# Performance work log

Hardware: AMD Instinct MI355X
Metric: run time of the kernel (lower is better)

Reference implementation:

```python
import math
import jax, jax.numpy as jnp
import numpy as np

B, Q, K, D = 32, 1024, 1024, 128
MASK_VALUE = -1000000.0


def setup_inputs() -> dict:
    key = jax.random.key(0)
    kq, kk, kv, kl = jax.random.split(key, 4)
    return {
        "queries": jax.random.normal(kq, (B, Q, D), dtype=jnp.float32),
        "keys": jax.random.normal(kk, (B, K, D), dtype=jnp.float32),
        "values": jax.random.normal(kv, (B, K, D), dtype=jnp.float32),
        "valid_lens": jax.random.randint(kl, (B,), 1, K + 1, dtype=jnp.int32),
    }


def reference(queries, keys, values, valid_lens):
    d = queries.shape[-1]
    # scores: [B, Q, K]
    scores = jnp.einsum("bqd,bkd->bqk", queries, keys) / math.sqrt(d)
    # key-padding mask: position k valid iff k < valid_lens[b] (broadcast over queries)
    mask = jnp.arange(keys.shape[1])[None, None, :] < valid_lens[:, None, None]
    scores = jnp.where(mask, scores, MASK_VALUE)
    attn = jax.nn.softmax(scores, axis=-1)
    # dropout p=0.0 -> identity
    return jnp.einsum("bqk,bkv->bqv", attn, values)
```

## Files before the change

kernel.cpp:

```cpp
#include <hip/hip_runtime.h>
#include <math.h>

typedef _Float16 f16;
typedef __attribute__((ext_vector_type(8))) _Float16 f16x8;
typedef __attribute__((ext_vector_type(4))) _Float16 f16x4;
typedef __attribute__((ext_vector_type(4))) float f32x4;

constexpr int BATCH = 32;
constexpr int QL = 1024;
constexpr int KL = 1024;
constexpr int D = 128;
constexpr int BQ = 64;
constexpr int BK = 64;
constexpr int CT = 8;
constexpr int DKP = 136;
constexpr int BKP = 72;

#define CSC 0.12752863187087177f

static __device__ __forceinline__ f16x4 pk4(float x, float y, float z, float w) {
  auto a = __builtin_amdgcn_cvt_pkrtz(x, y);
  auto b = __builtin_amdgcn_cvt_pkrtz(z, w);
  f16x4 h;
  h[0] = (f16)a[0]; h[1] = (f16)a[1]; h[2] = (f16)b[0]; h[3] = (f16)b[1];
  return h;
}
static __device__ __forceinline__ f16x8 pk8(float4 u, float4 v) {
  f16x4 a = pk4(u.x, u.y, u.z, u.w);
  f16x4 b = pk4(v.x, v.y, v.z, v.w);
  f16x8 h;
  h[0] = a[0]; h[1] = a[1]; h[2] = a[2]; h[3] = a[3];
  h[4] = b[0]; h[5] = b[1]; h[6] = b[2]; h[7] = b[3];
  return h;
}
static __device__ __forceinline__ f16x8 pk8v(f32x4 a, f32x4 b) {
  auto x0 = __builtin_amdgcn_cvt_pkrtz(a[0], a[1]);
  auto x1 = __builtin_amdgcn_cvt_pkrtz(a[2], a[3]);
  auto x2 = __builtin_amdgcn_cvt_pkrtz(b[0], b[1]);
  auto x3 = __builtin_amdgcn_cvt_pkrtz(b[2], b[3]);
  f16x8 h;
  h[0] = x0[0]; h[1] = x0[1]; h[2] = x1[0]; h[3] = x1[1];
  h[4] = x2[0]; h[5] = x2[1]; h[6] = x3[0]; h[7] = x3[1];
  return h;
}
static __device__ __forceinline__ f16x8 pk8s(float4 u, float4 v) {
  float4 a = {u.x * CSC, u.y * CSC, u.z * CSC, u.w * CSC};
  float4 b = {v.x * CSC, v.y * CSC, v.z * CSC, v.w * CSC};
  return pk8(a, b);
}

static __device__ __forceinline__ int krp(int kk) {
  return ((kk >> 5) << 5) | (((kk >> 2) & 1) << 4) | (((kk >> 3) & 3) << 2) | (kk & 3);
}

#define ISSUE(KR, VR, T)                                                   \
  do {                                                                     \
    const float4* Kt = (const float4*)(Kb + (size_t)(T) * BK * D);         \
    _Pragma("unroll")                                                      \
    for (int i_ = 0; i_ < 4; ++i_) {                                       \
      int cc_ = tid + i_ * 256;                                            \
      int row_ = cc_ >> 4, d04_ = (cc_ & 15) * 2;                          \
      KR[2 * i_]     = Kt[row_ * 32 + d04_];                               \
      KR[2 * i_ + 1] = Kt[row_ * 32 + d04_ + 1];                           \
    }                                                                      \
    const float* Vt = Vb + (size_t)(T) * BK * D;                           \
    _Pragma("unroll")                                                      \
    for (int i_ = 0; i_ < 2; ++i_) {                                       \
      int f_ = tid + i_ * 256;                                             \
      const float* base_ = Vt + (size_t)((f_ & 15) * 4) * D + (f_ >> 4) * 4; \
      VR[i_ * 4 + 0] = *(const float4*)(base_);                            \
      VR[i_ * 4 + 1] = *(const float4*)(base_ + D);                        \
      VR[i_ * 4 + 2] = *(const float4*)(base_ + 2 * D);                    \
      VR[i_ * 4 + 3] = *(const float4*)(base_ + 3 * D);                    \
    }                                                                      \
  } while (0)

#define DRAIN(KR, VR)                                                      \
  do {                                                                     \
    _Pragma("unroll")                                                      \
    for (int i_ = 0; i_ < 4; ++i_) {                                       \
      int cc_ = tid + i_ * 256;                                            \
      int row_ = cc_ >> 4, d0_ = (cc_ & 15) * 8;                           \
      *(f16x8*)&sK[krp(row_)][d0_] = pk8(KR[2 * i_], KR[2 * i_ + 1]);      \
    }                                                                      \
    _Pragma("unroll")                                                      \
    for (int i_ = 0; i_ < 2; ++i_) {                                       \
      int f_ = tid + i_ * 256;                                             \
      int k0_ = (f_ & 15) * 4, d0_ = (f_ >> 4) * 4;                        \
      float4 r0_ = VR[i_*4+0], r1_ = VR[i_*4+1], r2_ = VR[i_*4+2], r3_ = VR[i_*4+3]; \
      *(f16x4*)&sVT[d0_ + 0][k0_] = pk4(r0_.x, r1_.x, r2_.x, r3_.x);       \
      *(f16x4*)&sVT[d0_ + 1][k0_] = pk4(r0_.y, r1_.y, r2_.y, r3_.y);       \
      *(f16x4*)&sVT[d0_ + 2][k0_] = pk4(r0_.z, r1_.z, r2_.z, r3_.z);       \
      *(f16x4*)&sVT[d0_ + 3][k0_] = pk4(r0_.w, r1_.w, r2_.w, r3_.w);       \
    }                                                                      \
  } while (0)

#define TILE_BARRIER()                                                     \
  do {                                                                     \
    asm volatile("s_waitcnt lgkmcnt(0)" ::: "memory");                     \
    __builtin_amdgcn_s_barrier();                                          \
    asm volatile("" ::: "memory");                                         \
  } while (0)

__global__ __launch_bounds__(256, 2)
void attn_fwd(const float* __restrict__ Qp, const float* __restrict__ Kp,
              const float* __restrict__ Vp, const int* __restrict__ VLp,
              float* __restrict__ Op, float* __restrict__ wsO,
              float* __restrict__ wsL, int nks) {
  __shared__ f16 sK[BK][DKP];
  __shared__ f16 sVT[D][BKP];
  __shared__ int sN[32];
  __shared__ int sI[32];
  __shared__ int sCost[8];
  __shared__ int sCls[8];

  const int tid  = threadIdx.x;
  const int wave = tid >> 6, lane = tid & 63;
  const int l16  = lane & 15, quad = lane >> 4;

  if (tid < 32) sN[tid] = (VLp[tid] + BK - 1) / BK;
  __syncthreads();
  if (tid < 32) {
    int nb = sN[tid], r = 0;
    #pragma unroll
    for (int k = 0; k < 32; ++k) {
      int nk = sN[k];
      r += (nk > nb) || (nk == nb && k < tid);
    }
    sI[r] = tid;
  }
  __syncthreads();

  const int xcd = blockIdx.x & 7;
  const int j   = (int)blockIdx.x >> 3;

  int b, qt, ks, t0, t1, nt, vl;
  if (nks == 2) {
    if (tid < 8) {
      int lb = tid >> 1, kss = tid & 1;
      int gr = (lb == 0) ? xcd : (lb == 1) ? (15 - xcd)
             : (lb == 2) ? (16 + xcd) : (31 - xcd);
      int ntb = sN[sI[gr]];
      sCost[tid] = kss ? max(ntb - CT, 0) : min(ntb, CT);
    }
    __syncthreads();
    if (tid < 8) {
      int c = sCost[tid], r = 0;
      #pragma unroll
      for (int k = 0; k < 8; ++k)
        r += (sCost[k] > c) || (sCost[k] == c && k < tid);
      sCls[r] = tid;
    }
    __syncthreads();
    const int slot = j >> 5, c31 = j & 31;
    const int r = (slot == 0) ? c31 : (slot == 1) ? (63 - c31)
                : (slot == 2) ? (64 + c31) : (127 - c31);
    const int cls = sCls[r >> 4];
    const int lb = cls >> 1;
    ks = cls & 1;
    qt = r & 15;
    const int gr = (lb == 0) ? xcd : (lb == 1) ? (15 - xcd)
                 : (lb == 2) ? (16 + xcd) : (31 - xcd);
    b  = sI[gr];
    vl = VLp[b];
    nt = (vl + BK - 1) / BK;
    t0 = ks * CT;
    t1 = min(nt, ks * CT + CT);
    if (t0 >= t1) return;
  } else {
    const int jj = (j < 32) ? j : (95 - j);
    const int lr = jj >> 4;
    qt = jj & 15;
    ks = 0;
    const int gr = (lr == 0) ? xcd : (lr == 1) ? (15 - xcd)
                 : (lr == 2) ? (16 + xcd) : (31 - xcd);
    b  = sI[gr];
    vl = VLp[b];
    nt = (vl + BK - 1) / BK;
    t0 = 0; t1 = nt;
  }

  const float* Kb = Kp + (size_t)b * KL * D;
  const float* Vb = Vp + (size_t)b * KL * D;

  float4 kreg[8], vreg[8];

  const float* Qb = Qp + ((size_t)(b * QL + qt * BQ + wave * 16 + l16)) * D;
  float4 qtmp[8];
  #pragma unroll
  for (int kc = 0; kc < 4; ++kc) {
    const float* p = Qb + kc * 32 + quad * 8;
    qtmp[2 * kc]     = *(const float4*)p;
    qtmp[2 * kc + 1] = *(const float4*)(p + 4);
  }

  ISSUE(kreg, vreg, t0);

  f16x8 qf[4];
  #pragma unroll
  for (int kc = 0; kc < 4; ++kc) qf[kc] = pk8s(qtmp[2 * kc], qtmp[2 * kc + 1]);

  float lsum = 0.f;
  f32x4 o[8];
  #pragma unroll
  for (int dt = 0; dt < 8; ++dt) o[dt] = (f32x4){0.f, 0.f, 0.f, 0.f};

  for (int t = t0; t < t1; ++t) {
    TILE_BARRIER();
    DRAIN(kreg, vreg);
    if (t + 1 < t1) ISSUE(kreg, vreg, t + 1);
    TILE_BARRIER();

    f32x4 sv[4];
    #pragma unroll
    for (int ct = 0; ct < 4; ++ct) {
      f32x4 cacc = (f32x4){0.f, 0.f, 0.f, 0.f};
      #pragma unroll
      for (int kc = 0; kc < 4; ++kc) {
        f16x8 kf = *(const f16x8*)&sK[ct * 16 + l16][kc * 32 + quad * 8];
        cacc = __builtin_amdgcn_mfma_f32_16x16x32_f16(kf, qf[kc], cacc, 0, 0, 0);
      }
      sv[ct] = cacc;
    }

    if (t * BK + BK > vl) {
      #pragma unroll
      for (int ct = 0; ct < 4; ++ct) {
        int kb = t * BK + (ct >> 1) * 32 + (ct & 1) * 4 + quad * 8;
        #pragma unroll
        for (int r = 0; r < 4; ++r)
          sv[ct][r] = (kb + r) < vl ? sv[ct][r] : -1.0e9f;
      }
    }

    #pragma unroll
    for (int ct = 0; ct < 4; ++ct) {
      #pragma unroll
      for (int r = 0; r < 4; ++r) {
        float p = __builtin_amdgcn_exp2f(sv[ct][r]);
        sv[ct][r] = p;
        lsum += p;
      }
    }
    f16x8 pf0 = pk8v(sv[0], sv[1]);
    f16x8 pf1 = pk8v(sv[2], sv[3]);

    #pragma unroll
    for (int dt = 0; dt < 8; ++dt) {
      f16x8 vf0 = *(const f16x8*)&sVT[dt * 16 + l16][quad * 8];
      o[dt] = __builtin_amdgcn_mfma_f32_16x16x32_f16(vf0, pf0, o[dt], 0, 0, 0);
      f16x8 vf1 = *(const f16x8*)&sVT[dt * 16 + l16][32 + quad * 8];
      o[dt] = __builtin_amdgcn_mfma_f32_16x16x32_f16(vf1, pf1, o[dt], 0, 0, 0);
    }
  }

  float ls = lsum;
  ls += __shfl_xor(ls, 16);
  ls += __shfl_xor(ls, 32);

  if (nks == 1 || nt <= CT) {
    float* Ob = Op + ((size_t)(b * QL + qt * BQ + wave * 16)) * D;
    const float inv = 1.0f / ls;
    #pragma unroll
    for (int dt = 0; dt < 8; ++dt) {
      float4 w = {o[dt][0] * inv, o[dt][1] * inv, o[dt][2] * inv, o[dt][3] * inv};
      *(float4*)&Ob[(size_t)l16 * D + dt * 16 + quad * 4] = w;
    }
  } else {
    const int pair = b * 16 + qt;
    float* dst = (ks == 0)
        ? Op + ((size_t)(b * QL + qt * BQ + wave * 16)) * D
        : wsO + (size_t)pair * BQ * D + (size_t)(wave * 16) * D;
    #pragma unroll
    for (int dt = 0; dt < 8; ++dt) {
      float4 w = {o[dt][0], o[dt][1], o[dt][2], o[dt][3]};
      *(float4*)&dst[(size_t)l16 * D + dt * 16 + quad * 4] = w;
    }
    if (quad == 0) wsL[(pair * 2 + ks) * 64 + wave * 16 + l16] = ls;
  }
}

__global__ __launch_bounds__(256)
void attn_combine(float* __restrict__ Op, const float* __restrict__ wsO,
                  const float* __restrict__ wsL, const int* __restrict__ VLp) {
  const int pair = blockIdx.x;
  const int b = pair >> 4;
  if (VLp[b] <= CT * BK) return;
  float* Ob = Op + ((size_t)(b * QL + (pair & 15) * BQ)) * D;
  const float* o1 = wsO + (size_t)pair * BQ * D;
  const float* Lt = wsL + pair * 128;
  const int tid = threadIdx.x;
  #pragma unroll
  for (int i = 0; i < 8; ++i) {
    int fi = tid + i * 256;
    int row = fi >> 5;
    float inv = 1.0f / (Lt[row] + Lt[64 + row]);
    float4 a = ((const float4*)Ob)[fi];
    float4 c = ((const float4*)o1)[fi];
    float4 w = {(a.x + c.x) * inv, (a.y + c.y) * inv,
                (a.z + c.z) * inv, (a.w + c.w) * inv};
    ((float4*)Ob)[fi] = w;
  }
}

extern "C" void kernel_launch(void* const* d_in, const int* in_sizes, int n_in,
                              void* d_out, int out_size, void* d_ws, size_t ws_size,
                              hipStream_t stream) {
  const float* Qp = (const float*)d_in[0];
  const float* Kp = (const float*)d_in[1];
  const float* Vp = (const float*)d_in[2];
  const int*   VL = (const int*)d_in[3];
  float* Op = (float*)d_out;

  const size_t n_pairs = (size_t)BATCH * (QL / BQ);
  const size_t need = n_pairs * BQ * D * 4 + n_pairs * 128 * 4;
  if (d_ws != nullptr && ws_size >= need) {
    float* wsO = (float*)d_ws;
    float* wsL = (float*)d_ws + n_pairs * BQ * D;
    attn_fwd<<<dim3(2 * (int)n_pairs), dim3(256), 0, stream>>>(
        Qp, Kp, Vp, VL, Op, wsO, wsL, 2);
    attn_combine<<<dim3((int)n_pairs), dim3(256), 0, stream>>>(Op, wsO, wsL, VL);
  } else {
    attn_fwd<<<dim3((int)n_pairs), dim3(256), 0, stream>>>(
        Qp, Kp, Vp, VL, Op, nullptr, nullptr, 1);
  }
}
```

Before: 124.9 us.

## Generalize split-K to four key chunks and drop cost-sorted block scheduling

Generalizes the flash-attention key split from a fixed two chunks to a runtime count (four when the workspace allows), each block covering 16/nks key tiles, and the combine kernel sums a variable number of partial outputs and row sums. It also replaces the per-block cost ranking of (batch, split) classes with a plain index mapping. The aim is finer-grained work units, so that batches with very different valid lengths balance better across CUs. In exchange the combine pass reads more workspace traffic and many more, smaller blocks are launched, most of which exit early.

```diff
diff --git a/kernel.cpp b/kernel.cpp
--- a/kernel.cpp
+++ b/kernel.cpp
@@ -12,7 +12,6 @@
 constexpr int D = 128;
 constexpr int BQ = 64;
 constexpr int BK = 64;
-constexpr int CT = 8;
 constexpr int DKP = 136;
 constexpr int BKP = 72;
 
@@ -111,12 +110,11 @@
   __shared__ f16 sVT[D][BKP];
   __shared__ int sN[32];
   __shared__ int sI[32];
-  __shared__ int sCost[8];
-  __shared__ int sCls[8];
 
   const int tid  = threadIdx.x;
   const int wave = tid >> 6, lane = tid & 63;
   const int l16  = lane & 15, quad = lane >> 4;
+  const int ctk  = 16 / nks;
 
   if (tid < 32) sN[tid] = (VLp[tid] + BK - 1) / BK;
   __syncthreads();
@@ -135,37 +133,17 @@
   const int j   = (int)blockIdx.x >> 3;
 
   int b, qt, ks, t0, t1, nt, vl;
-  if (nks == 2) {
-    if (tid < 8) {
-      int lb = tid >> 1, kss = tid & 1;
-      int gr = (lb == 0) ? xcd : (lb == 1) ? (15 - xcd)
-             : (lb == 2) ? (16 + xcd) : (31 - xcd);
-      int ntb = sN[sI[gr]];
-      sCost[tid] = kss ? max(ntb - CT, 0) : min(ntb, CT);
-    }
-    __syncthreads();
-    if (tid < 8) {
-      int c = sCost[tid], r = 0;
-      #pragma unroll
-      for (int k = 0; k < 8; ++k)
-        r += (sCost[k] > c) || (sCost[k] == c && k < tid);
-      sCls[r] = tid;
-    }
-    __syncthreads();
-    const int slot = j >> 5, c31 = j & 31;
-    const int r = (slot == 0) ? c31 : (slot == 1) ? (63 - c31)
-                : (slot == 2) ? (64 + c31) : (127 - c31);
-    const int cls = sCls[r >> 4];
-    const int lb = cls >> 1;
-    ks = cls & 1;
-    qt = r & 15;
+  if (nks >= 2) {
+    ks = j >> 6;
+    const int lb = (j >> 4) & 3;
+    qt = j & 15;
     const int gr = (lb == 0) ? xcd : (lb == 1) ? (15 - xcd)
                  : (lb == 2) ? (16 + xcd) : (31 - xcd);
     b  = sI[gr];
     vl = VLp[b];
     nt = (vl + BK - 1) / BK;
-    t0 = ks * CT;
-    t1 = min(nt, ks * CT + CT);
+    t0 = ks * ctk;
+    t1 = min(nt, t0 + ctk);
     if (t0 >= t1) return;
   } else {
     const int jj = (j < 32) ? j : (95 - j);
@@ -258,7 +236,7 @@
   ls += __shfl_xor(ls, 16);
   ls += __shfl_xor(ls, 32);
 
-  if (nks == 1 || nt <= CT) {
+  if (nks == 1 || nt <= ctk) {
     float* Ob = Op + ((size_t)(b * QL + qt * BQ + wave * 16)) * D;
     const float inv = 1.0f / ls;
     #pragma unroll
@@ -270,35 +248,45 @@
     const int pair = b * 16 + qt;
     float* dst = (ks == 0)
         ? Op + ((size_t)(b * QL + qt * BQ + wave * 16)) * D
-        : wsO + (size_t)pair * BQ * D + (size_t)(wave * 16) * D;
+        : wsO + ((size_t)pair * (nks - 1) + (ks - 1)) * BQ * D
+              + (size_t)(wave * 16) * D;
     #pragma unroll
     for (int dt = 0; dt < 8; ++dt) {
       float4 w = {o[dt][0], o[dt][1], o[dt][2], o[dt][3]};
       *(float4*)&dst[(size_t)l16 * D + dt * 16 + quad * 4] = w;
     }
-    if (quad == 0) wsL[(pair * 2 + ks) * 64 + wave * 16 + l16] = ls;
+    if (quad == 0) wsL[(pair * nks + ks) * 64 + wave * 16 + l16] = ls;
   }
 }
 
 __global__ __launch_bounds__(256)
 void attn_combine(float* __restrict__ Op, const float* __restrict__ wsO,
-                  const float* __restrict__ wsL, const int* __restrict__ VLp) {
+                  const float* __restrict__ wsL, const int* __restrict__ VLp,
+                  int nks) {
   const int pair = blockIdx.x;
   const int b = pair >> 4;
-  if (VLp[b] <= CT * BK) return;
+  const int ctk = 16 / nks;
+  const int nt = (VLp[b] + BK - 1) / BK;
+  if (nt <= ctk) return;
+  const int nch = (nt + ctk - 1) / ctk;
   float* Ob = Op + ((size_t)(b * QL + (pair & 15) * BQ)) * D;
-  const float* o1 = wsO + (size_t)pair * BQ * D;
-  const float* Lt = wsL + pair * 128;
+  const float* Lt = wsL + (size_t)pair * nks * 64;
   const int tid = threadIdx.x;
   #pragma unroll
   for (int i = 0; i < 8; ++i) {
     int fi = tid + i * 256;
     int row = fi >> 5;
-    float inv = 1.0f / (Lt[row] + Lt[64 + row]);
+    float l = Lt[row];
+    for (int p = 1; p < nch; ++p) l += Lt[p * 64 + row];
+    float inv = 1.0f / l;
     float4 a = ((const float4*)Ob)[fi];
-    float4 c = ((const float4*)o1)[fi];
-    float4 w = {(a.x + c.x) * inv, (a.y + c.y) * inv,
-                (a.z + c.z) * inv, (a.w + c.w) * inv};
+    for (int p = 1; p < nch; ++p) {
+      const float4* o1 = (const float4*)(wsO +
+          ((size_t)pair * (nks - 1) + (p - 1)) * BQ * D);
+      float4 c = o1[fi];
+      a.x += c.x; a.y += c.y; a.z += c.z; a.w += c.w;
+    }
+    float4 w = {a.x * inv, a.y * inv, a.z * inv, a.w * inv};
     ((float4*)Ob)[fi] = w;
   }
 }
@@ -313,13 +301,20 @@
   float* Op = (float*)d_out;
 
   const size_t n_pairs = (size_t)BATCH * (QL / BQ);
-  const size_t need = n_pairs * BQ * D * 4 + n_pairs * 128 * 4;
-  if (d_ws != nullptr && ws_size >= need) {
+  int nks = 1;
+  for (int cand = 4; cand >= 2; cand >>= 1) {
+    size_t need = n_pairs * (size_t)(cand - 1) * BQ * D * 4
+                + n_pairs * (size_t)cand * 64 * 4;
+    if (d_ws != nullptr && ws_size >= need) { nks = cand; break; }
+  }
+
+  if (nks > 1) {
     float* wsO = (float*)d_ws;
-    float* wsL = (float*)d_ws + n_pairs * BQ * D;
-    attn_fwd<<<dim3(2 * (int)n_pairs), dim3(256), 0, stream>>>(
-        Qp, Kp, Vp, VL, Op, wsO, wsL, 2);
-    attn_combine<<<dim3((int)n_pairs), dim3(256), 0, stream>>>(Op, wsO, wsL, VL);
+    float* wsL = (float*)d_ws + n_pairs * (size_t)(nks - 1) * BQ * D;
+    attn_fwd<<<dim3((int)n_pairs * nks), dim3(256), 0, stream>>>(
+        Qp, Kp, Vp, VL, Op, wsO, wsL, nks);
+    attn_combine<<<dim3((int)n_pairs), dim3(256), 0, stream>>>(
+        Op, wsO, wsL, VL, nks);
   } else {
     attn_fwd<<<dim3((int)n_pairs), dim3(256), 0, stream>>>(
         Qp, Kp, Vp, VL, Op, nullptr, nullptr, 1);
```

New measurement: 141.9 us. 1.14x slower.

## Double-buffer K/V shared tiles and simplify split-K block scheduling

Applied to the files above, without the earlier changes.

Doubles the LDS buffers for K and transposed V so the next tile is drained into the alternate buffer after computing on the current one, cutting the per-tile barriers from two to one. It also removes the cost-sorted class assignment for the two-way key split and maps blocks directly to split, batch slot and query tile, dropping two block-wide syncs. Doubling LDS usage may lower occupancy under the two-blocks-per-CU launch bound, and the simpler mapping may balance work across XCDs less evenly.

```diff
diff --git a/kernel.cpp b/kernel.cpp
--- a/kernel.cpp
+++ b/kernel.cpp
@@ -75,23 +75,23 @@
     }                                                                      \
   } while (0)
 
-#define DRAIN(KR, VR)                                                      \
+#define DRAIN(KR, VR, NB)                                                  \
   do {                                                                     \
     _Pragma("unroll")                                                      \
     for (int i_ = 0; i_ < 4; ++i_) {                                       \
       int cc_ = tid + i_ * 256;                                            \
       int row_ = cc_ >> 4, d0_ = (cc_ & 15) * 8;                           \
-      *(f16x8*)&sK[krp(row_)][d0_] = pk8(KR[2 * i_], KR[2 * i_ + 1]);      \
+      *(f16x8*)&sK[NB][krp(row_)][d0_] = pk8(KR[2 * i_], KR[2 * i_ + 1]);  \
     }                                                                      \
     _Pragma("unroll")                                                      \
     for (int i_ = 0; i_ < 2; ++i_) {                                       \
       int f_ = tid + i_ * 256;                                             \
       int k0_ = (f_ & 15) * 4, d0_ = (f_ >> 4) * 4;                        \
       float4 r0_ = VR[i_*4+0], r1_ = VR[i_*4+1], r2_ = VR[i_*4+2], r3_ = VR[i_*4+3]; \
-      *(f16x4*)&sVT[d0_ + 0][k0_] = pk4(r0_.x, r1_.x, r2_.x, r3_.x);       \
-      *(f16x4*)&sVT[d0_ + 1][k0_] = pk4(r0_.y, r1_.y, r2_.y, r3_.y);       \
-      *(f16x4*)&sVT[d0_ + 2][k0_] = pk4(r0_.z, r1_.z, r2_.z, r3_.z);       \
-      *(f16x4*)&sVT[d0_ + 3][k0_] = pk4(r0_.w, r1_.w, r2_.w, r3_.w);       \
+      *(f16x4*)&sVT[NB][d0_ + 0][k0_] = pk4(r0_.x, r1_.x, r2_.x, r3_.x);   \
+      *(f16x4*)&sVT[NB][d0_ + 1][k0_] = pk4(r0_.y, r1_.y, r2_.y, r3_.y);   \
+      *(f16x4*)&sVT[NB][d0_ + 2][k0_] = pk4(r0_.z, r1_.z, r2_.z, r3_.z);   \
+      *(f16x4*)&sVT[NB][d0_ + 3][k0_] = pk4(r0_.w, r1_.w, r2_.w, r3_.w);   \
     }                                                                      \
   } while (0)
 
@@ -107,12 +107,10 @@
               const float* __restrict__ Vp, const int* __restrict__ VLp,
               float* __restrict__ Op, float* __restrict__ wsO,
               float* __restrict__ wsL, int nks) {
-  __shared__ f16 sK[BK][DKP];
-  __shared__ f16 sVT[D][BKP];
+  __shared__ f16 sK[2][BK][DKP];
+  __shared__ f16 sVT[2][D][BKP];
   __shared__ int sN[32];
   __shared__ int sI[32];
-  __shared__ int sCost[8];
-  __shared__ int sCls[8];
 
   const int tid  = threadIdx.x;
   const int wave = tid >> 6, lane = tid & 63;
@@ -136,36 +134,16 @@
 
   int b, qt, ks, t0, t1, nt, vl;
   if (nks == 2) {
-    if (tid < 8) {
-      int lb = tid >> 1, kss = tid & 1;
-      int gr = (lb == 0) ? xcd : (lb == 1) ? (15 - xcd)
-             : (lb == 2) ? (16 + xcd) : (31 - xcd);
-      int ntb = sN[sI[gr]];
-      sCost[tid] = kss ? max(ntb - CT, 0) : min(ntb, CT);
-    }
-    __syncthreads();
-    if (tid < 8) {
-      int c = sCost[tid], r = 0;
-      #pragma unroll
-      for (int k = 0; k < 8; ++k)
-        r += (sCost[k] > c) || (sCost[k] == c && k < tid);
-      sCls[r] = tid;
-    }
-    __syncthreads();
-    const int slot = j >> 5, c31 = j & 31;
-    const int r = (slot == 0) ? c31 : (slot == 1) ? (63 - c31)
-                : (slot == 2) ? (64 + c31) : (127 - c31);
-    const int cls = sCls[r >> 4];
-    const int lb = cls >> 1;
-    ks = cls & 1;
-    qt = r & 15;
+    ks = j >> 6;
+    const int lb = (j >> 4) & 3;
+    qt = j & 15;
     const int gr = (lb == 0) ? xcd : (lb == 1) ? (15 - xcd)
                  : (lb == 2) ? (16 + xcd) : (31 - xcd);
     b  = sI[gr];
     vl = VLp[b];
     nt = (vl + BK - 1) / BK;
     t0 = ks * CT;
-    t1 = min(nt, ks * CT + CT);
+    t1 = min(nt, t0 + CT);
     if (t0 >= t1) return;
   } else {
     const int jj = (j < 32) ? j : (95 - j);
@@ -205,11 +183,14 @@
   #pragma unroll
   for (int dt = 0; dt < 8; ++dt) o[dt] = (f32x4){0.f, 0.f, 0.f, 0.f};
 
+  DRAIN(kreg, vreg, 0);
+  TILE_BARRIER();
+
   for (int t = t0; t < t1; ++t) {
-    TILE_BARRIER();
-    DRAIN(kreg, vreg);
-    if (t + 1 < t1) ISSUE(kreg, vreg, t + 1);
-    TILE_BARRIER();
+    const int cur = (t - t0) & 1, nxt = cur ^ 1;
+    const bool more = (t + 1 < t1);
+
+    if (more) ISSUE(kreg, vreg, t + 1);
 
     f32x4 sv[4];
     #pragma unroll
@@ -217,7 +198,7 @@
       f32x4 cacc = (f32x4){0.f, 0.f, 0.f, 0.f};
       #pragma unroll
       for (int kc = 0; kc < 4; ++kc) {
-        f16x8 kf = *(const f16x8*)&sK[ct * 16 + l16][kc * 32 + quad * 8];
+        f16x8 kf = *(const f16x8*)&sK[cur][ct * 16 + l16][kc * 32 + quad * 8];
         cacc = __builtin_amdgcn_mfma_f32_16x16x32_f16(kf, qf[kc], cacc, 0, 0, 0);
       }
       sv[ct] = cacc;
@@ -247,11 +228,14 @@
 
     #pragma unroll
     for (int dt = 0; dt < 8; ++dt) {
-      f16x8 vf0 = *(const f16x8*)&sVT[dt * 16 + l16][quad * 8];
+      f16x8 vf0 = *(const f16x8*)&sVT[cur][dt * 16 + l16][quad * 8];
       o[dt] = __builtin_amdgcn_mfma_f32_16x16x32_f16(vf0, pf0, o[dt], 0, 0, 0);
-      f16x8 vf1 = *(const f16x8*)&sVT[dt * 16 + l16][32 + quad * 8];
+      f16x8 vf1 = *(const f16x8*)&sVT[cur][dt * 16 + l16][32 + quad * 8];
       o[dt] = __builtin_amdgcn_mfma_f32_16x16x32_f16(vf1, pf1, o[dt], 0, 0, 0);
     }
+
+    if (more) DRAIN(kreg, vreg, nxt);
+    TILE_BARRIER();
   }
 
   float ls = lsum;
```

After: 127.2 us. About the same (+1.8%).
